# Kernel optimization log

Measured on AMD Instinct MI355X. Metric: run time of the kernel, lower is better.

## Reference

```python
import jax, jax.numpy as jnp
import numpy as np

KERNEL_MUL = 2.0
KERNEL_NUM = 5


def setup_inputs() -> dict:
    key = jax.random.key(0)
    k1, k2 = jax.random.split(key)
    source = jax.random.normal(k1, (4096, 1024), dtype=jnp.float32)
    target = jax.random.normal(k2, (4096, 1024), dtype=jnp.float32)
    return {"source": source, "target": target}


def _mmd_rbf(source, target):
    n_src = source.shape[0]
    total = jnp.concatenate([source, target], axis=0)  # [2N, D]
    n = total.shape[0]
    # pairwise squared L2 via the matmul identity: |a-b|^2 = |a|^2 + |b|^2 - 2 a.b
    sq = jnp.sum(total * total, axis=1)  # [2N]
    l2 = jnp.maximum(sq[:, None] + sq[None, :] - 2.0 * (total @ total.T), 0.0)  # [2N, 2N]
    # bandwidth from detached distances (torch uses l2_distance.data)
    denom = max(1, n * n - n)
    bandwidth = jax.lax.stop_gradient(jnp.sum(l2)) / denom
    bandwidth = bandwidth / (KERNEL_MUL ** (KERNEL_NUM // 2))
    kernels = jnp.zeros_like(l2)
    for i in range(KERNEL_NUM):  # fixed small loop over bandwidths
        kernels = kernels + jnp.exp(-l2 / (bandwidth * (KERNEL_MUL ** i)))
    xx = jnp.mean(kernels[:n_src, :n_src])
    yy = jnp.mean(kernels[n_src:, n_src:])
    xy = jnp.mean(kernels[:n_src, n_src:])
    yx = jnp.mean(kernels[n_src:, :n_src])
    return xx + yy - xy - yx


def reference(source, target):
    return _mmd_rbf(source, target)
```

## Files before the change

kernel.cpp:

```cpp
#include <hip/hip_runtime.h>

typedef float f32x4 __attribute__((ext_vector_type(4)));
typedef int i32x4v __attribute__((ext_vector_type(4)));
typedef int i32x8 __attribute__((ext_vector_type(8)));

#define N_HALF 4096
#define NT 8192
#define D 1024
#define TILE 128
#define NBLK 2080

#define WS_TB_OFF 0
#define WS_SQQ_OFF (NT * D)
#define WS_SQE_OFF (WS_SQQ_OFF + NT * 4)
#define WS_COLPART_OFF (WS_SQE_OFF + NT * 4)
#define WS_COLSUM2_OFF (WS_COLPART_OFF + 512 * D * 4)

struct BlockMap {
  unsigned short by[NBLK];
  unsigned short bx[NBLK];
  constexpr BlockMap() : by(), bx() {
    const int G[8][5] = {{17, 18, 19, 21, -1}, {22, 23, 24, 25, -1},
                         {26, 28, 29, 30, -1}, {31, 32, 33, 34, -1},
                         {0, 1, 2, 3, 4},      {5, 6, 7, 8, 9},
                         {10, 11, 12, 14, 20}, {13, 15, 16, 27, 35}};
    unsigned short sby[8][264] = {}, sbx[8][264] = {};
    int len[8] = {};
    for (int x = 0; x < 8; ++x)
      for (int gi = 0; gi < 5; ++gi) {
        int s = G[x][gi];
        if (s < 0) continue;
        int SX = 0;
        while ((SX + 1) * (SX + 2) / 2 <= s) ++SX;
        int SY = s - SX * (SX + 1) / 2;
        for (int u = 0; u < 8; ++u)
          for (int v = 0; v < 8; ++v) {
            int r = 8 * SY + u, c = 8 * SX + v;
            if (r <= c) {
              sby[x][len[x]] = (unsigned short)r;
              sbx[x][len[x]] = (unsigned short)c;
              ++len[x];
            }
          }
      }
    unsigned short pby[64] = {}, pbx[64] = {};
    int ns = 0;
    for (int x = 0; x < 8; ++x)
      for (int j = 260; j < len[x]; ++j) { pby[ns] = sby[x][j]; pbx[ns] = sbx[x][j]; ++ns; }
    int sp = 0;
    for (int x = 0; x < 8; ++x)
      for (int j = 0; j < 260; ++j) {
        int b = 8 * j + x;
        if (j < len[x]) { by[b] = sby[x][j]; bx[b] = sbx[x][j]; }
        else { by[b] = pby[sp]; bx[b] = pbx[sp]; ++sp; }
      }
  }
};
__constant__ BlockMap d_bmap = BlockMap();

__device__ __forceinline__ float wave_sum(float v) {
#pragma unroll
  for (int off = 32; off > 0; off >>= 1) v += __shfl_xor(v, off, 64);
  return v;
}

__device__ __forceinline__ float fast_exp2(float x) {
#if __has_builtin(__builtin_amdgcn_exp2f)
  return __builtin_amdgcn_exp2f(x);
#else
  return exp2f(x);
#endif
}

__device__ __forceinline__ void load_lds16(const void* gptr, void* ldsptr) {
  __builtin_amdgcn_global_load_lds(
      (const __attribute__((address_space(1))) void*)gptr,
      (__attribute__((address_space(3))) void*)ldsptr, 16, 0, 0);
}

__global__ __launch_bounds__(256) void prep_kernel(const float* __restrict__ src,
                                                   const float* __restrict__ tgt,
                                                   unsigned int* __restrict__ tb8,
                                                   float* __restrict__ sqq,
                                                   float* __restrict__ sqe,
                                                   float* __restrict__ colpart,
                                                   float* __restrict__ out) {
  if (blockIdx.x == 0 && threadIdx.x == 0) out[0] = 0.f;
  int w = threadIdx.x >> 6, lane = threadIdx.x & 63;
  int rbase = blockIdx.x * 16 + w * 4;
  f32x4 csum[4] = {};
#pragma unroll
  for (int r = 0; r < 4; ++r) {
    int row = rbase + r;
    const float* rowp = (row < N_HALF) ? (src + (size_t)row * D)
                                       : (tgt + (size_t)(row - N_HALF) * D);
    float accq = 0.f, acce = 0.f;
#pragma unroll
    for (int i = 0; i < 4; ++i) {
      int v4 = i * 64 + lane;
      float4 v = ((const float4*)rowp)[v4];
      int pk = __builtin_amdgcn_cvt_pk_fp8_f32(v.x, v.y, 0, false);
      pk = __builtin_amdgcn_cvt_pk_fp8_f32(v.z, v.w, pk, true);
      tb8[(size_t)row * 256 + v4] = (unsigned int)pk;
      float q0 = __builtin_amdgcn_cvt_f32_fp8(pk, 0);
      float q1 = __builtin_amdgcn_cvt_f32_fp8(pk, 1);
      float q2 = __builtin_amdgcn_cvt_f32_fp8(pk, 2);
      float q3 = __builtin_amdgcn_cvt_f32_fp8(pk, 3);
      accq = fmaf(q0, q0, accq); accq = fmaf(q1, q1, accq);
      accq = fmaf(q2, q2, accq); accq = fmaf(q3, q3, accq);
      acce = fmaf(v.x, v.x, acce); acce = fmaf(v.y, v.y, acce);
      acce = fmaf(v.z, v.z, acce); acce = fmaf(v.w, v.w, acce);
      csum[i][0] += v.x; csum[i][1] += v.y; csum[i][2] += v.z; csum[i][3] += v.w;
    }
    accq = wave_sum(accq);
    acce = wave_sum(acce);
    if (lane == 0) { sqq[row] = accq; sqe[row] = acce; }
  }
  __shared__ f32x4 cred[4][256];
#pragma unroll
  for (int i = 0; i < 4; ++i) cred[w][i * 64 + lane] = csum[i];
  __syncthreads();
  int t = threadIdx.x;
  f32x4 s = cred[0][t] + cred[1][t] + cred[2][t] + cred[3][t];
  ((f32x4*)colpart)[(size_t)blockIdx.x * 256 + t] = s;
}

__global__ __launch_bounds__(256) void colred_kernel(const float* __restrict__ colpart,
                                                     const float* __restrict__ sqe,
                                                     float* __restrict__ colsum2) {
  int b = blockIdx.x, t = threadIdx.x;
  __shared__ float red[256];
  if (b < 256) {
    int c = b * 4 + (t & 3);
    float s = 0.f;
    for (int p = (t >> 2); p < 512; p += 64) s += colpart[(size_t)p * D + c];
    red[t] = s;
    __syncthreads();
    if (t < 4) {
      float cs = 0.f;
      for (int g = 0; g < 64; ++g) cs += red[g * 4 + t];
      red[t] = cs * cs;
    }
    __syncthreads();
    if (t == 0) colsum2[b] = red[0] + red[1] + red[2] + red[3];
  } else {
    float s = 0.f;
    for (int k = 0; k < 32; ++k) s += sqe[t + 256 * k];
    s = wave_sum(s);
    if ((t & 63) == 0) red[t >> 6] = s;
    __syncthreads();
    if (t == 0) colsum2[256] = red[0] + red[1] + red[2] + red[3];
  }
}

__global__ __launch_bounds__(256, 3) void mmd_gemm(const unsigned char* __restrict__ tb8,
                                                   const float* __restrict__ sqq,
                                                   const float* __restrict__ colsum2,
                                                   float* __restrict__ out) {
  int bid = blockIdx.x;
  int by = d_bmap.by[bid], bx = d_bmap.bx[bid];
  __shared__ __align__(16) char As[TILE * 128];
  __shared__ __align__(16) char Bs[TILE * 128];
  int tid = threadIdx.x, w = tid >> 6, lane = tid & 63;
  int wy = w >> 1, wx = w & 1;
  int rowBase = by * TILE, colBase = bx * TILE;

  float part = 0.f;
#pragma unroll
  for (int k2 = 0; k2 < 4; ++k2) part += colsum2[lane + 64 * k2];
  part = wave_sum(part);
  float ssqf = colsum2[256];
  double suml2 = 2.0 * 8192.0 * (double)ssqf - 2.0 * (double)part;
  double band = suml2 / (8192.0 * 8191.0) / 4.0;
  float c4 = (float)(-1.4426950408889634 / (band * 16.0));

  f32x4 acc[4][4] = {};
  int l8 = lane >> 3, lc = lane & 7, swz = lc ^ l8;
  const char* tbb = (const char*)tb8;
  size_t ag = (size_t)(rowBase + 32 * w + l8) * 1024 + (size_t)swz * 16;
  size_t bg = (size_t)(colBase + 32 * w + l8) * 1024 + (size_t)swz * 16;
  char* Asl = As + w * 4096;
  char* Bsl = Bs + w * 4096;

  int r16 = lane & 15, q = lane >> 4, rx7 = lane & 7;
  int arowb = (wy * 64 + r16) * 128;
  int browb = (wx * 64 + r16) * 128;
  int ch0 = ((2 * q) ^ rx7) * 16;
  int ch1 = ((2 * q + 1) ^ rx7) * 16;

  for (int kk = 0; kk < 8; ++kk) {
    size_t ko = (size_t)kk * 128;
#pragma unroll
    for (int j = 0; j < 4; ++j) {
      load_lds16(tbb + ag + ko + (size_t)j * 8192, Asl + j * 1024);
      load_lds16(tbb + bg + ko + (size_t)j * 8192, Bsl + j * 1024);
    }
    __syncthreads();
    i32x8 af[4], bf[4];
#pragma unroll
    for (int mt = 0; mt < 4; ++mt) {
      const char* p = As + arowb + mt * 2048;
      i32x4v lo = *(const i32x4v*)(p + ch0);
      i32x4v hi = *(const i32x4v*)(p + ch1);
      af[mt] = (i32x8){lo[0], lo[1], lo[2], lo[3], hi[0], hi[1], hi[2], hi[3]};
    }
#pragma unroll
    for (int nt = 0; nt < 4; ++nt) {
      const char* p = Bs + browb + nt * 2048;
      i32x4v lo = *(const i32x4v*)(p + ch0);
      i32x4v hi = *(const i32x4v*)(p + ch1);
      bf[nt] = (i32x8){lo[0], lo[1], lo[2], lo[3], hi[0], hi[1], hi[2], hi[3]};
    }
#pragma unroll
    for (int mt = 0; mt < 4; ++mt)
#pragma unroll
      for (int nt = 0; nt < 4; ++nt)
        acc[mt][nt] = __builtin_amdgcn_mfma_scale_f32_16x16x128_f8f6f4(
            af[mt], bf[nt], acc[mt][nt], 0, 0, 0, 0x7f7f7f7f, 0, 0x7f7f7f7f);
    __syncthreads();
  }

  int colg = colBase + wx * 64 + r16;
  int rquad = q * 4;
  float sqc[4];
#pragma unroll
  for (int nt = 0; nt < 4; ++nt) sqc[nt] = sqq[colg + nt * 16];
  float wsum = 0.f;
#pragma unroll
  for (int mt = 0; mt < 4; ++mt) {
    int rb = rowBase + wy * 64 + mt * 16 + rquad;
    float srs[4] = {sqq[rb], sqq[rb + 1], sqq[rb + 2], sqq[rb + 3]};
#pragma unroll
    for (int nt = 0; nt < 4; ++nt) {
      f32x4 v = acc[mt][nt];
#pragma unroll
      for (int r = 0; r < 4; ++r) {
        float l2 = fmaxf(fmaf(-2.f, v[r], srs[r] + sqc[nt]), 0.f);
        float tt = fast_exp2(l2 * c4);
        float t2 = tt * tt, t4 = t2 * t2, t8 = t4 * t4, t16 = t8 * t8;
        wsum += ((tt + t2) + (t4 + t8)) + t16;
      }
    }
  }
  wsum = wave_sum(wsum);
  float* redA = (float*)As;
  if (lane == 0) redA[w] = wsum;
  __syncthreads();
  if (tid == 0) {
    float sgn = ((by < 32) == (bx < 32)) ? 1.f : -1.f;
    float wgt = (bx == by) ? 1.f : 2.f;
    float val = (redA[0] + redA[1] + redA[2] + redA[3]) * sgn * wgt *
                (1.f / 16777216.f);
    atomicAdd(out, val);
  }
}

extern "C" void kernel_launch(void* const* d_in, const int* in_sizes, int n_in,
                              void* d_out, int out_size, void* d_ws, size_t ws_size,
                              hipStream_t stream) {
  (void)in_sizes; (void)n_in; (void)out_size; (void)ws_size;
  const float* src = (const float*)d_in[0];
  const float* tgt = (const float*)d_in[1];
  char* ws = (char*)d_ws;
  unsigned int* tb8 = (unsigned int*)(ws + WS_TB_OFF);
  float* sqq = (float*)(ws + WS_SQQ_OFF);
  float* sqe = (float*)(ws + WS_SQE_OFF);
  float* colpart = (float*)(ws + WS_COLPART_OFF);
  float* colsum2 = (float*)(ws + WS_COLSUM2_OFF);
  float* out = (float*)d_out;

  prep_kernel<<<512, 256, 0, stream>>>(src, tgt, tb8, sqq, sqe, colpart, out);
  colred_kernel<<<257, 256, 0, stream>>>(colpart, sqe, colsum2);
  mmd_gemm<<<NBLK, 256, 0, stream>>>((const unsigned char*)tb8, sqq, colsum2, out);
}
```

Before: 136.8 us.

## Load FP8 fragments directly from global into registers, drop LDS staging

Result: slower. 217.6 us (+59.1%).

```diff
diff --git a/kernel.cpp b/kernel.cpp
--- a/kernel.cpp
+++ b/kernel.cpp
@@ -15,6 +15,7 @@
 #define WS_SQE_OFF (WS_SQQ_OFF + NT * 4)
 #define WS_COLPART_OFF (WS_SQE_OFF + NT * 4)
 #define WS_COLSUM2_OFF (WS_COLPART_OFF + 512 * D * 4)
+#define WS_PARTIAL_OFF (WS_COLSUM2_OFF + 2048)
 
 struct BlockMap {
   unsigned short by[NBLK];
@@ -72,10 +73,10 @@
 #endif
 }
 
-__device__ __forceinline__ void load_lds16(const void* gptr, void* ldsptr) {
-  __builtin_amdgcn_global_load_lds(
-      (const __attribute__((address_space(1))) void*)gptr,
-      (__attribute__((address_space(3))) void*)ldsptr, 16, 0, 0);
+__device__ __forceinline__ i32x8 ld8(const char* p) {
+  i32x4v lo = *(const i32x4v*)p;
+  i32x4v hi = *(const i32x4v*)(p + 16);
+  return (i32x8){lo[0], lo[1], lo[2], lo[3], hi[0], hi[1], hi[2], hi[3]};
 }
 
 __global__ __launch_bounds__(256) void prep_kernel(const float* __restrict__ src,
@@ -83,9 +84,7 @@
                                                    unsigned int* __restrict__ tb8,
                                                    float* __restrict__ sqq,
                                                    float* __restrict__ sqe,
-                                                   float* __restrict__ colpart,
-                                                   float* __restrict__ out) {
-  if (blockIdx.x == 0 && threadIdx.x == 0) out[0] = 0.f;
+                                                   float* __restrict__ colpart) {
   int w = threadIdx.x >> 6, lane = threadIdx.x & 63;
   int rbase = blockIdx.x * 16 + w * 4;
   f32x4 csum[4] = {};
@@ -153,14 +152,12 @@
   }
 }
 
-__global__ __launch_bounds__(256, 3) void mmd_gemm(const unsigned char* __restrict__ tb8,
+__global__ __launch_bounds__(256, 2) void mmd_gemm(const unsigned char* __restrict__ tb8,
                                                    const float* __restrict__ sqq,
                                                    const float* __restrict__ colsum2,
-                                                   float* __restrict__ out) {
+                                                   float* __restrict__ partial) {
   int bid = blockIdx.x;
   int by = d_bmap.by[bid], bx = d_bmap.bx[bid];
-  __shared__ __align__(16) char As[TILE * 128];
-  __shared__ __align__(16) char Bs[TILE * 128];
   int tid = threadIdx.x, w = tid >> 6, lane = tid & 63;
   int wy = w >> 1, wx = w & 1;
   int rowBase = by * TILE, colBase = bx * TILE;
@@ -174,50 +171,40 @@
   double band = suml2 / (8192.0 * 8191.0) / 4.0;
   float c4 = (float)(-1.4426950408889634 / (band * 16.0));
 
+  int r16 = lane & 15, q = lane >> 4;
+  const char* tbb = (const char*)tb8;
+  const char* ap = tbb + (size_t)(rowBase + wy * 64 + r16) * 1024 + q * 32;
+  const char* bp = tbb + (size_t)(colBase + wx * 64 + r16) * 1024 + q * 32;
+
   f32x4 acc[4][4] = {};
-  int l8 = lane >> 3, lc = lane & 7, swz = lc ^ l8;
-  const char* tbb = (const char*)tb8;
-  size_t ag = (size_t)(rowBase + 32 * w + l8) * 1024 + (size_t)swz * 16;
-  size_t bg = (size_t)(colBase + 32 * w + l8) * 1024 + (size_t)swz * 16;
-  char* Asl = As + w * 4096;
-  char* Bsl = Bs + w * 4096;
-
-  int r16 = lane & 15, q = lane >> 4, rx7 = lane & 7;
-  int arowb = (wy * 64 + r16) * 128;
-  int browb = (wx * 64 + r16) * 128;
-  int ch0 = ((2 * q) ^ rx7) * 16;
-  int ch1 = ((2 * q + 1) ^ rx7) * 16;
-
+  i32x8 cA[4], cB[4];
+#pragma unroll
+  for (int mt = 0; mt < 4; ++mt) cA[mt] = ld8(ap + mt * 16384);
+#pragma unroll
+  for (int nt = 0; nt < 4; ++nt) cB[nt] = ld8(bp + nt * 16384);
+
+#pragma unroll
   for (int kk = 0; kk < 8; ++kk) {
-    size_t ko = (size_t)kk * 128;
-#pragma unroll
-    for (int j = 0; j < 4; ++j) {
-      load_lds16(tbb + ag + ko + (size_t)j * 8192, Asl + j * 1024);
-      load_lds16(tbb + bg + ko + (size_t)j * 8192, Bsl + j * 1024);
-    }
-    __syncthreads();
-    i32x8 af[4], bf[4];
-#pragma unroll
-    for (int mt = 0; mt < 4; ++mt) {
-      const char* p = As + arowb + mt * 2048;
-      i32x4v lo = *(const i32x4v*)(p + ch0);
-      i32x4v hi = *(const i32x4v*)(p + ch1);
-      af[mt] = (i32x8){lo[0], lo[1], lo[2], lo[3], hi[0], hi[1], hi[2], hi[3]};
-    }
-#pragma unroll
-    for (int nt = 0; nt < 4; ++nt) {
-      const char* p = Bs + browb + nt * 2048;
-      i32x4v lo = *(const i32x4v*)(p + ch0);
-      i32x4v hi = *(const i32x4v*)(p + ch1);
-      bf[nt] = (i32x8){lo[0], lo[1], lo[2], lo[3], hi[0], hi[1], hi[2], hi[3]};
+    i32x8 nA[4], nB[4];
+    if (kk < 7) {
+      int ko = (kk + 1) * 128;
+#pragma unroll
+      for (int mt = 0; mt < 4; ++mt) nA[mt] = ld8(ap + mt * 16384 + ko);
+#pragma unroll
+      for (int nt = 0; nt < 4; ++nt) nB[nt] = ld8(bp + nt * 16384 + ko);
     }
 #pragma unroll
     for (int mt = 0; mt < 4; ++mt)
 #pragma unroll
       for (int nt = 0; nt < 4; ++nt)
         acc[mt][nt] = __builtin_amdgcn_mfma_scale_f32_16x16x128_f8f6f4(
-            af[mt], bf[nt], acc[mt][nt], 0, 0, 0, 0x7f7f7f7f, 0, 0x7f7f7f7f);
-    __syncthreads();
+            cA[mt], cB[nt], acc[mt][nt], 0, 0, 0, 0x7f7f7f7f, 0, 0x7f7f7f7f);
+    if (kk < 7) {
+#pragma unroll
+      for (int mt = 0; mt < 4; ++mt) cA[mt] = nA[mt];
+#pragma unroll
+      for (int nt = 0; nt < 4; ++nt) cB[nt] = nB[nt];
+    }
   }
 
   int colg = colBase + wx * 64 + r16;
@@ -243,16 +230,30 @@
     }
   }
   wsum = wave_sum(wsum);
-  float* redA = (float*)As;
-  if (lane == 0) redA[w] = wsum;
+  __shared__ float redw[4];
+  if (lane == 0) redw[w] = wsum;
   __syncthreads();
   if (tid == 0) {
     float sgn = ((by < 32) == (bx < 32)) ? 1.f : -1.f;
     float wgt = (bx == by) ? 1.f : 2.f;
-    float val = (redA[0] + redA[1] + redA[2] + redA[3]) * sgn * wgt *
-                (1.f / 16777216.f);
-    atomicAdd(out, val);
-  }
+    partial[bid] = (redw[0] + redw[1] + redw[2] + redw[3]) * sgn * wgt;
+  }
+}
+
+__global__ void finalize_kernel(const float* __restrict__ partial, float* __restrict__ out) {
+  int t = threadIdx.x;
+  double s = 0.0;
+  for (int k = 0; k < 9; ++k) {
+    int i = t + 256 * k;
+    if (i < NBLK) s += (double)partial[i];
+  }
+#pragma unroll
+  for (int off = 32; off > 0; off >>= 1) s += __shfl_xor(s, off, 64);
+  __shared__ double red[4];
+  if ((t & 63) == 0) red[t >> 6] = s;
+  __syncthreads();
+  if (t == 0) out[0] = (float)((red[0] + red[1] + red[2] + red[3]) /
+                               ((double)N_HALF * (double)N_HALF));
 }
 
 extern "C" void kernel_launch(void* const* d_in, const int* in_sizes, int n_in,
@@ -267,9 +268,10 @@
   float* sqe = (float*)(ws + WS_SQE_OFF);
   float* colpart = (float*)(ws + WS_COLPART_OFF);
   float* colsum2 = (float*)(ws + WS_COLSUM2_OFF);
-  float* out = (float*)d_out;
-
-  prep_kernel<<<512, 256, 0, stream>>>(src, tgt, tb8, sqq, sqe, colpart, out);
+  float* partial = (float*)(ws + WS_PARTIAL_OFF);
+
+  prep_kernel<<<512, 256, 0, stream>>>(src, tgt, tb8, sqq, sqe, colpart);
   colred_kernel<<<257, 256, 0, stream>>>(colpart, sqe, colsum2);
-  mmd_gemm<<<NBLK, 256, 0, stream>>>((const unsigned char*)tb8, sqq, colsum2, out);
-}
+  mmd_gemm<<<NBLK, 256, 0, stream>>>((const unsigned char*)tb8, sqq, colsum2, partial);
+  finalize_kernel<<<1, 256, 0, stream>>>(partial, (float*)d_out);
+}
```
